# Optimization experiments

Measured on AMD Instinct MI355X. Metric: run time of the kernel, lower is better.

## Reference

```python
import math
import jax, jax.numpy as jnp
import numpy as np

B, T, C = 2, 2048, 2048
H, G = 16, 4
D = C // H  # head_dim = 128
KV = G * D
SOFT_CAP = 50.0
EPS = 1e-6


def setup_inputs() -> dict:
    key = jax.random.key(0)
    ks = jax.random.split(key, 5)
    s = 1.0 / math.sqrt(C)
    return {
        "x": jax.random.normal(ks[0], (B, T, C), jnp.float32),
        "Wq": jax.random.normal(ks[1], (C, C), jnp.float32) * s,
        "Wk": jax.random.normal(ks[2], (KV, C), jnp.float32) * s,
        "Wv": jax.random.normal(ks[3], (KV, C), jnp.float32) * s,
        "Wo": jax.random.normal(ks[4], (C, C), jnp.float32) * s,
        "bo": jnp.zeros((C,), jnp.float32),
        "q_norm_w": jnp.ones((D,), jnp.float32),
        "k_norm_w": jnp.ones((D,), jnp.float32),
    }


def _rmsnorm(x, w):
    # norm/sqrt(d) formulation, eps added to rms (matches torch module exactly)
    rms = jnp.linalg.norm(x, axis=-1, keepdims=True) / math.sqrt(x.shape[-1])
    return w * (x / (rms + EPS))


def _rotary_tables(seq_len, dim):
    inv_freq = 1.0 / (10000.0 ** (jnp.arange(0, dim, 2, dtype=jnp.float32) / dim))
    t = jnp.arange(seq_len, dtype=jnp.float32)
    freqs = jnp.outer(t, inv_freq)  # [T, D/2]
    return jnp.cos(freqs), jnp.sin(freqs)


def _apply_rope(x, cos, sin):
    # x: [B, T, h, D]; cos/sin: [T, D/2] broadcast as [1, T, 1, D/2]
    d = x.shape[-1] // 2
    x1, x2 = x[..., :d], x[..., d:]
    c = cos[None, :, None, :]
    s = sin[None, :, None, :]
    return jnp.concatenate([x1 * c + x2 * s, -x1 * s + x2 * c], axis=-1)


def reference(x, Wq, Wk, Wv, Wo, bo, q_norm_w, k_norm_w):
    b, t, c = x.shape
    q = (x @ Wq.T).reshape(b, t, H, D)
    k = (x @ Wk.T).reshape(b, t, G, D)
    v = (x @ Wv.T).reshape(b, t, G, D)

    cos, sin = _rotary_tables(t, D)
    q = _apply_rope(_rmsnorm(q, q_norm_w), cos, sin)
    k = _apply_rope(_rmsnorm(k, k_norm_w), cos, sin)

    q = q.transpose(0, 2, 1, 3)              # [B, H, T, D]
    k = jnp.repeat(k.transpose(0, 2, 1, 3), H // G, axis=1)  # [B, H, T, D]
    v = jnp.repeat(v.transpose(0, 2, 1, 3), H // G, axis=1)

    att = jnp.einsum("bhqd,bhkd->bhqk", q, k) / math.sqrt(D)
    causal = jnp.tril(jnp.ones((t, t), bool))
    att = jnp.where(causal[None, None], att, -jnp.inf)
    att = SOFT_CAP * jnp.tanh(att / SOFT_CAP)  # masked entries -> -50
    att = jax.nn.softmax(att, axis=-1)

    y = jnp.einsum("bhqk,bhkd->bhqd", att, v)
    y = y.transpose(0, 2, 1, 3).reshape(b, t, c)
    return y @ Wo.T + bo
```

## Files before the change

### kernel.cpp

```cpp
#include <hip/hip_runtime.h>
#include <math.h>

#define T_SEQ 2048
#define C_DIM 2048
#define NH    16
#define NG    4
#define DH    128
#define BATCH 2

typedef unsigned short u16;
typedef __bf16 bf16_t;
typedef bf16_t bf16x8 __attribute__((ext_vector_type(8)));
typedef float  f32x4  __attribute__((ext_vector_type(4)));

static __device__ __forceinline__ u16 f2bf(float f) {
    return __builtin_bit_cast(u16, (__bf16)f);
}

static __device__ __forceinline__ void gll16(const void* g, void* lds) {
    __builtin_amdgcn_global_load_lds(
        (const __attribute__((address_space(1))) void*)(unsigned long long)(g),
        (__attribute__((address_space(3))) void*)(unsigned int)(unsigned long long)(lds),
        16, 0, 0);
}

__global__ __launch_bounds__(256)
void cast_multi(const float* __restrict__ x,  const float* __restrict__ wq,
                const float* __restrict__ wk, const float* __restrict__ wv,
                u16* __restrict__ xo, u16* __restrict__ wqo,
                u16* __restrict__ wko, u16* __restrict__ wvo) {
    int i = blockIdx.x * 256 + threadIdx.x;
    const float* src; u16* dst; int off;
    if (i < 1048576)      { src = x;  dst = xo;  off = i; }
    else if (i < 1572864) { src = wq; dst = wqo; off = i - 1048576; }
    else if (i < 1703936) { src = wk; dst = wko; off = i - 1572864; }
    else                  { src = wv; dst = wvo; off = i - 1703936; }
    const float4* p = (const float4*)src + (size_t)off * 2;
    float4 a = p[0], b = p[1];
    u16 u[8] = {f2bf(a.x), f2bf(a.y), f2bf(a.z), f2bf(a.w),
                f2bf(b.x), f2bf(b.y), f2bf(b.z), f2bf(b.w)};
    *(uint4*)(dst + (size_t)off * 8) = *(const uint4*)u;
}

__global__ __launch_bounds__(256)
void cast_f32_bf16(const float* __restrict__ in, u16* __restrict__ out, int n8) {
    int i = blockIdx.x * 256 + threadIdx.x;
    if (i >= n8) return;
    const float4* p = (const float4*)in + (size_t)i * 2;
    float4 a = p[0], b = p[1];
    u16 u[8] = {f2bf(a.x), f2bf(a.y), f2bf(a.z), f2bf(a.w),
                f2bf(b.x), f2bf(b.y), f2bf(b.z), f2bf(b.w)};
    *(uint4*)(out + (size_t)i * 8) = *(const uint4*)u;
}

__global__ __launch_bounds__(256)
void rope_tables(float* __restrict__ cosT, float* __restrict__ sinT) {
    int i = blockIdx.x * 256 + threadIdx.x;
    int tp = i >> 6, ln = i & 63;
    float invfreq = __builtin_amdgcn_exp2f(-(float)ln * (13.287712379549449f / 64.0f));
    float s, c;
    sincosf((float)tp * invfreq, &s, &c);
    cosT[i] = c;
    sinT[i] = s;
}

static __device__ __forceinline__ void gemm_body(
        u16* As, u16* Bs,
        const u16* __restrict__ A, const u16* __restrict__ B,
        const float* __restrict__ bias, float* __restrict__ C,
        int N, int K, int m0, int n0) {
    const int t    = threadIdx.x;
    const int lane = t & 63, w = t >> 6;
    const int l15  = lane & 15, quad = lane >> 4;
    const int wr   = w >> 1, wc = w & 1;

    f32x4 acc[4][4];
#pragma unroll
    for (int mt = 0; mt < 4; ++mt)
#pragma unroll
        for (int nt = 0; nt < 4; ++nt) acc[mt][nt] = (f32x4){0.f, 0.f, 0.f, 0.f};

    const int off0 = w*2048 + lane*16;
    const int r0 = off0 >> 6,          c0 = (off0 & 63) >> 1;
    const int r1 = (off0+1024) >> 6,   c1 = ((off0+1024) & 63) >> 1;
    const u16* Ag0 = A + (size_t)(m0 + r0) * K + c0;
    const u16* Ag1 = A + (size_t)(m0 + r1) * K + c1;
    const u16* Bg0 = B + (size_t)(n0 + r0) * K + c0;
    const u16* Bg1 = B + (size_t)(n0 + r1) * K + c1;
    char* AsB = (char*)As; char* BsB = (char*)Bs;
    const int ldsOff0 = w*2048, ldsOff1 = w*2048 + 1024;

    for (int k0 = 0; k0 < K; k0 += 32) {
        gll16(Ag0 + k0, AsB + ldsOff0);
        gll16(Ag1 + k0, AsB + ldsOff1);
        gll16(Bg0 + k0, BsB + ldsOff0);
        gll16(Bg1 + k0, BsB + ldsOff1);
        __syncthreads();
        bf16x8 af[4], bf[4];
#pragma unroll
        for (int mt = 0; mt < 4; ++mt)
            af[mt] = __builtin_bit_cast(bf16x8,
                *(const uint4*)&As[(wr*64 + mt*16 + l15)*32 + quad*8]);
#pragma unroll
        for (int nt = 0; nt < 4; ++nt)
            bf[nt] = __builtin_bit_cast(bf16x8,
                *(const uint4*)&Bs[(wc*64 + nt*16 + l15)*32 + quad*8]);
#pragma unroll
        for (int mt = 0; mt < 4; ++mt)
#pragma unroll
            for (int nt = 0; nt < 4; ++nt)
                acc[mt][nt] = __builtin_amdgcn_mfma_f32_16x16x32_bf16(
                                  af[mt], bf[nt], acc[mt][nt], 0, 0, 0);
        __syncthreads();
    }

#pragma unroll
    for (int mt = 0; mt < 4; ++mt)
#pragma unroll
        for (int nt = 0; nt < 4; ++nt) {
            const int col = n0 + wc*64 + nt*16 + l15;
            const float bv = bias ? bias[col] : 0.f;
#pragma unroll
            for (int r = 0; r < 4; ++r) {
                const int row = m0 + wr*64 + mt*16 + quad*4 + r;
                C[(size_t)row * N + col] = acc[mt][nt][r] + bv;
            }
        }
}

__global__ __launch_bounds__(256)
void gemm_nt_bf16(const u16* __restrict__ A, const u16* __restrict__ B,
                  const float* __restrict__ bias, float* __restrict__ C,
                  int N, int K) {
    __shared__ __align__(16) u16 As[128*32];
    __shared__ __align__(16) u16 Bs[128*32];
    gemm_body(As, Bs, A, B, bias, C, N, K, blockIdx.y*128, blockIdx.x*128);
}

__global__ __launch_bounds__(256)
void gemm_qkv(const u16* __restrict__ A,  const u16* __restrict__ Bq,
              const u16* __restrict__ Bk, const u16* __restrict__ Bv,
              float* __restrict__ Cq, float* __restrict__ Ck, float* __restrict__ Cv) {
    __shared__ __align__(16) u16 As[128*32];
    __shared__ __align__(16) u16 Bs[128*32];
    const int bx = blockIdx.x;
    const u16* B; float* C; int N, n0;
    if (bx < 16)      { B = Bq; C = Cq; N = 2048; n0 = bx * 128; }
    else if (bx < 20) { B = Bk; C = Ck; N = 512;  n0 = (bx-16) * 128; }
    else              { B = Bv; C = Cv; N = 512;  n0 = (bx-20) * 128; }
    gemm_body(As, Bs, A, B, nullptr, C, N, 2048, blockIdx.y*128, n0);
}

__global__ __launch_bounds__(256)
void rmsnorm_rope_qk(const float* __restrict__ qf, const float* __restrict__ kf,
                     const float* __restrict__ qw, const float* __restrict__ kw,
                     const float* __restrict__ cosT, const float* __restrict__ sinT,
                     u16* __restrict__ qo, u16* __restrict__ ko) {
    const int blk  = blockIdx.x;
    const int sub  = threadIdx.x >> 6;
    const int lane = threadIdx.x & 63;
    const float* in; const float* w; u16* out; int row, nheads; float scale;
    if (blk < 16384) {
        in = qf; w = qw; out = qo; nheads = NH; scale = 0.08838834764831845f;
        row = blk * 4 + sub;
    } else {
        in = kf; w = kw; out = ko; nheads = NG; scale = 1.0f;
        row = (blk - 16384) * 4 + sub;
    }
    const float* p = in + (size_t)row * 128;
    float x1 = p[lane], x2 = p[lane + 64];
    float ss = x1*x1 + x2*x2;
#pragma unroll
    for (int off = 32; off >= 1; off >>= 1) ss += __shfl_xor(ss, off, 64);
    float inv = 1.0f / (sqrtf(ss * (1.0f/128.0f)) + 1e-6f);
    float x1n = w[lane]      * x1 * inv;
    float x2n = w[lane + 64] * x2 * inv;
    int tpos = (row / nheads) & (T_SEQ - 1);
    float c = cosT[tpos*64 + lane];
    float s = sinT[tpos*64 + lane];
    out[(size_t)row*128 + lane]      = f2bf((x1n * c + x2n * s) * scale);
    out[(size_t)row*128 + lane + 64] = f2bf((x2n * c - x1n * s) * scale);
}

__global__ __launch_bounds__(256)
void v_cast_transpose(const float* __restrict__ v, u16* __restrict__ vt) {
    __shared__ u16 Lt[128 * 66];
    const int t  = threadIdx.x;
    const int t0 = blockIdx.x * 64;
    const int bg = blockIdx.y;
    const int b  = bg / NG, g = bg % NG;
#pragma unroll
    for (int rep = 0; rep < 8; ++rep) {
        int idx = rep * 256 + t;
        int i   = idx >> 5;
        int c   = idx & 31;
        float4 f = *(const float4*)(v + ((size_t)(b*T_SEQ + t0 + i)*NG + g)*DH + c*4);
        Lt[(c*4+0)*66 + i] = f2bf(f.x);
        Lt[(c*4+1)*66 + i] = f2bf(f.y);
        Lt[(c*4+2)*66 + i] = f2bf(f.z);
        Lt[(c*4+3)*66 + i] = f2bf(f.w);
    }
    __syncthreads();
#pragma unroll
    for (int rep = 0; rep < 4; ++rep) {
        int idx = rep * 256 + t;
        int d = idx >> 3, c = idx & 7;
        const u16* src = &Lt[d*66 + c*8];
        uint4 val;
        val.x = *(const unsigned int*)(src + 0);
        val.y = *(const unsigned int*)(src + 2);
        val.z = *(const unsigned int*)(src + 4);
        val.w = *(const unsigned int*)(src + 6);
        *(uint4*)(vt + ((size_t)(bg*DH + d))*T_SEQ + t0 + c*8) = val;
    }
}

__global__ __launch_bounds__(256, 2)
void flash_attn_mfma(const u16* __restrict__ qh, const u16* __restrict__ kh,
                     const u16* __restrict__ vt, u16* __restrict__ y) {
    __shared__ __align__(16) u16 Ks[2][64*128];
    __shared__ __align__(16) u16 Vs[2][128*64];
    __shared__ __align__(16) u16 Ps[64*64];

    const int t    = threadIdx.x;
    const int lane = t & 63, w = t >> 6;
    const int l15  = lane & 15, quad = lane >> 4;
    const int bid  = blockIdx.x;
    const int bg   = bid & 7;
    const int b    = bg >> 2, g = bg & 3;
    const int cidx = bid >> 3;
    const int chunk = b ? cidx : (63 - cidx);
    const int q0   = chunk * 32;
    const int h    = g * (NH / NG) + w;

    const float C0 =  1.4426950408889634f;
    const float C1 = -0.48089834696298777f;
    const float C2 =  0.19235933878519512f;
    const float C3 = -0.07785972536301652f;

    bf16x8 aq[2][4];
#pragma unroll
    for (int m = 0; m < 2; ++m) {
        const u16* qp = qh + ((size_t)(b*T_SEQ + q0 + m*16 + l15) * NH + h) * DH;
#pragma unroll
        for (int kc = 0; kc < 4; ++kc)
            aq[m][kc] = __builtin_bit_cast(bf16x8, *(const uint4*)(qp + kc*32 + quad*8));
    }

    f32x4 accO[2][8];
#pragma unroll
    for (int m = 0; m < 2; ++m)
#pragma unroll
        for (int nd = 0; nd < 8; ++nd) accO[m][nd] = (f32x4){0.f, 0.f, 0.f, 0.f};
    float ls[2][4] = {{0.f,0.f,0.f,0.f},{0.f,0.f,0.f,0.f}};

    const u16* kgb = kh + ((size_t)b*T_SEQ*NG + g)*DH;
    const u16* vgb = vt + ((size_t)(b*NG + g)*DH)*T_SEQ;

    const int krb = t >> 4, kcl = t & 15;
    const int vdb = t >> 3, vcl = t & 7;

    const int ktiles = q0/64 + 1;

#pragma unroll
    for (int j = 0; j < 4; ++j) {
        const int kr = j*16 + krb;
        gll16(kgb + (size_t)kr*(NG*DH) + ((kcl ^ (kr & 7)) << 3),
              (char*)Ks[0] + j*4096 + w*1024);
        const int vd = j*32 + vdb;
        gll16(vgb + (size_t)vd*T_SEQ + ((vcl ^ (vd & 7)) << 3),
              (char*)Vs[0] + j*4096 + w*1024);
    }

    for (int kt = 0; kt < ktiles; ++kt) {
        asm volatile("s_waitcnt vmcnt(0)" ::: "memory");
        __syncthreads();

        if (kt + 1 < ktiles) {
            const int k0n = (kt + 1) * 64, bn = (kt + 1) & 1;
#pragma unroll
            for (int j = 0; j < 4; ++j) {
                const int kr = j*16 + krb;
                gll16(kgb + (size_t)(k0n + kr)*(NG*DH) + ((kcl ^ (kr & 7)) << 3),
                      (char*)Ks[bn] + j*4096 + w*1024);
                const int vd = j*32 + vdb;
                gll16(vgb + (size_t)vd*T_SEQ + k0n + ((vcl ^ (vd & 7)) << 3),
                      (char*)Vs[bn] + j*4096 + w*1024);
            }
        }

        const u16* Kb = Ks[kt & 1];
        const u16* Vb = Vs[kt & 1];
        const int k0 = kt * 64;
        const bool diag = (kt == ktiles - 1);

        f32x4 accS[2][4];
#pragma unroll
        for (int m = 0; m < 2; ++m)
#pragma unroll
            for (int nt = 0; nt < 4; ++nt) accS[m][nt] = (f32x4){0.f,0.f,0.f,0.f};

        __builtin_amdgcn_s_setprio(1);
#pragma unroll
        for (int nt = 0; nt < 4; ++nt) {
            const int krow = nt*16 + l15;
            const int kswz = (krow & 7) << 3;
#pragma unroll
            for (int kc = 0; kc < 4; ++kc) {
                bf16x8 bk = __builtin_bit_cast(bf16x8,
                    *(const uint4*)&Kb[krow*128 + ((kc*32 + quad*8) ^ kswz)]);
                accS[0][nt] = __builtin_amdgcn_mfma_f32_16x16x32_bf16(aq[0][kc], bk, accS[0][nt], 0, 0, 0);
                accS[1][nt] = __builtin_amdgcn_mfma_f32_16x16x32_bf16(aq[1][kc], bk, accS[1][nt], 0, 0, 0);
            }
        }
        __builtin_amdgcn_s_setprio(0);

        bf16x8 ap[2][2];
#pragma unroll
        for (int m = 0; m < 2; ++m) {
#pragma unroll
            for (int nt = 0; nt < 4; ++nt) {
                const int colg = k0 + nt*16 + l15;
#pragma unroll
                for (int r = 0; r < 4; ++r) {
                    float sv = accS[m][nt][r];
                    float z = sv * 0.02f;
                    float u = z * z;
                    float poly = fmaf(u, fmaf(u, fmaf(u, C3, C2), C1), C0);
                    float pv = __builtin_amdgcn_exp2f(sv * poly);
                    if (diag) {
                        const int rowg = q0 + m*16 + quad*4 + r;
                        pv = (colg > rowg) ? 0.f : pv;
                    }
                    ls[m][r] += pv;
                    const int prow = w*16 + r*4 + quad;
                    const int pswz = ((quad << 1) | (r & 1)) << 3;
                    Ps[prow*64 + ((nt*16 + l15) ^ pswz)] = f2bf(pv);
                }
            }
            const int srow = (l15 & 3)*4 + (l15 >> 2);
            const int arow = w*16 + srow;
            const int aswz = (((l15 >> 2) << 1) | (l15 & 1)) << 3;
            ap[m][0] = __builtin_bit_cast(bf16x8,
                *(const uint4*)&Ps[arow*64 + ((quad*8)      ^ aswz)]);
            ap[m][1] = __builtin_bit_cast(bf16x8,
                *(const uint4*)&Ps[arow*64 + ((32 + quad*8) ^ aswz)]);
        }

        __builtin_amdgcn_s_setprio(1);
#pragma unroll
        for (int nd = 0; nd < 8; ++nd) {
            const int vrow = nd*16 + l15;
            const int vswz = (vrow & 7) << 3;
#pragma unroll
            for (int kc = 0; kc < 2; ++kc) {
                bf16x8 bv = __builtin_bit_cast(bf16x8,
                    *(const uint4*)&Vb[vrow*64 + ((kc*32 + quad*8) ^ vswz)]);
                accO[0][nd] = __builtin_amdgcn_mfma_f32_16x16x32_bf16(ap[0][kc], bv, accO[0][nd], 0, 0, 0);
                accO[1][nd] = __builtin_amdgcn_mfma_f32_16x16x32_bf16(ap[1][kc], bv, accO[1][nd], 0, 0, 0);
            }
        }
        __builtin_amdgcn_s_setprio(0);
    }

#pragma unroll
    for (int m = 0; m < 2; ++m)
#pragma unroll
        for (int r = 0; r < 4; ++r) {
            float v = ls[m][r];
            v += __shfl_xor(v, 1, 64);
            v += __shfl_xor(v, 2, 64);
            v += __shfl_xor(v, 4, 64);
            v += __shfl_xor(v, 8, 64);
            const float invl = 1.f / v;
            u16* yp = y + (size_t)(b*T_SEQ + q0 + m*16 + quad*4 + r) * C_DIM + h*DH;
#pragma unroll
            for (int nd = 0; nd < 8; ++nd)
                yp[nd*16 + l15] = f2bf(accO[m][nd][r] * invl);
        }
}

extern "C" void kernel_launch(void* const* d_in, const int* in_sizes, int n_in,
                              void* d_out, int out_size, void* d_ws, size_t ws_size,
                              hipStream_t stream) {
    const float* x  = (const float*)d_in[0];
    const float* Wq = (const float*)d_in[1];
    const float* Wk = (const float*)d_in[2];
    const float* Wv = (const float*)d_in[3];
    const float* Wo = (const float*)d_in[4];
    const float* bo = (const float*)d_in[5];
    const float* qw = (const float*)d_in[6];
    const float* kw = (const float*)d_in[7];
    float* out = (float*)d_out;

    const size_t qE = (size_t)BATCH * T_SEQ * NH * DH;
    const size_t kE = (size_t)BATCH * T_SEQ * NG * DH;
    const size_t wqE = (size_t)C_DIM * C_DIM;
    const size_t wkE = (size_t)(NG*DH) * C_DIM;

    float* qf  = (float*)d_ws;
    float* kf  = qf + qE;
    float* vf  = kf + kE;
    u16*   qh  = (u16*)(vf + kE);
    u16*   khb = qh + qE;
    u16*   vtb = khb + kE;
    u16*   xh  = vtb + kE;
    u16*   wqh = xh + qE;
    u16*   wkh = wqh + wqE;
    u16*   wvh = wkh + wkE;
    float* cosT = (float*)(wvh + wkE);
    float* sinT = cosT + 131072;
    u16*   woh = (u16*)kf;
    u16*   yh  = (u16*)qf;

    const int M = BATCH * T_SEQ;
    dim3 blk(256);

    rope_tables<<<dim3(512), blk, 0, stream>>>(cosT, sinT);

    cast_multi<<<dim3(7168), blk, 0, stream>>>(x, Wq, Wk, Wv, xh, wqh, wkh, wvh);

    gemm_qkv<<<dim3(24, M/128), blk, 0, stream>>>(xh, wqh, wkh, wvh, qf, kf, vf);

    rmsnorm_rope_qk<<<dim3(M*NH/4 + M*NG/4), blk, 0, stream>>>(qf, kf, qw, kw, cosT, sinT, qh, khb);
    v_cast_transpose<<<dim3(T_SEQ/64, BATCH*NG), blk, 0, stream>>>(vf, vtb);

    cast_f32_bf16<<<dim3(wqE/8/256), blk, 0, stream>>>(Wo, woh, wqE/8);

    flash_attn_mfma<<<dim3(512), blk, 0, stream>>>(qh, khb, vtb, yh);

    gemm_nt_bf16<<<dim3(C_DIM/128, M/128), blk, 0, stream>>>(yh, woh, bo, out, C_DIM, C_DIM);
}
```

Measured before the change: 343.8 us.

## Compute transposed S tiles so P stays in registers, removing the LDS round trip

```diff
diff --git a/kernel.cpp b/kernel.cpp
--- a/kernel.cpp
+++ b/kernel.cpp
@@ -220,16 +220,13 @@
                      const u16* __restrict__ vt, u16* __restrict__ y) {
     __shared__ __align__(16) u16 Ks[2][64*128];
     __shared__ __align__(16) u16 Vs[2][128*64];
-    __shared__ __align__(16) u16 Ps[64*64];
 
     const int t    = threadIdx.x;
     const int lane = t & 63, w = t >> 6;
     const int l15  = lane & 15, quad = lane >> 4;
-    const int bid  = blockIdx.x;
-    const int bg   = bid & 7;
+    const int bg   = blockIdx.y;
     const int b    = bg >> 2, g = bg & 3;
-    const int cidx = bid >> 3;
-    const int chunk = b ? cidx : (63 - cidx);
+    const int chunk = b ? (int)blockIdx.x : (63 - (int)blockIdx.x);
     const int q0   = chunk * 32;
     const int h    = g * (NH / NG) + w;
 
@@ -252,7 +249,7 @@
     for (int m = 0; m < 2; ++m)
 #pragma unroll
         for (int nd = 0; nd < 8; ++nd) accO[m][nd] = (f32x4){0.f, 0.f, 0.f, 0.f};
-    float ls[2][4] = {{0.f,0.f,0.f,0.f},{0.f,0.f,0.f,0.f}};
+    float ls[2] = {0.f, 0.f};
 
     const u16* kgb = kh + ((size_t)b*T_SEQ*NG + g)*DH;
     const u16* vgb = vt + ((size_t)(b*NG + g)*DH)*T_SEQ;
@@ -265,7 +262,9 @@
 #pragma unroll
     for (int j = 0; j < 4; ++j) {
         const int kr = j*16 + krb;
-        gll16(kgb + (size_t)kr*(NG*DH) + ((kcl ^ (kr & 7)) << 3),
+        const int rp = kr & 31;
+        const int kphys = (kr & 32) + ((rp >> 2) & 3)*8 + (rp >> 4)*4 + (rp & 3);
+        gll16(kgb + (size_t)kphys*(NG*DH) + ((kcl ^ (kr & 7)) << 3),
               (char*)Ks[0] + j*4096 + w*1024);
         const int vd = j*32 + vdb;
         gll16(vgb + (size_t)vd*T_SEQ + ((vcl ^ (vd & 7)) << 3),
@@ -281,7 +280,9 @@
 #pragma unroll
             for (int j = 0; j < 4; ++j) {
                 const int kr = j*16 + krb;
-                gll16(kgb + (size_t)(k0n + kr)*(NG*DH) + ((kcl ^ (kr & 7)) << 3),
+                const int rp = kr & 31;
+                const int kphys = (kr & 32) + ((rp >> 2) & 3)*8 + (rp >> 4)*4 + (rp & 3);
+                gll16(kgb + (size_t)(k0n + kphys)*(NG*DH) + ((kcl ^ (kr & 7)) << 3),
                       (char*)Ks[bn] + j*4096 + w*1024);
                 const int vd = j*32 + vdb;
                 gll16(vgb + (size_t)vd*T_SEQ + k0n + ((vcl ^ (vd & 7)) << 3),
@@ -294,85 +295,77 @@
         const int k0 = kt * 64;
         const bool diag = (kt == ktiles - 1);
 
-        f32x4 accS[2][4];
-#pragma unroll
-        for (int m = 0; m < 2; ++m)
-#pragma unroll
-            for (int nt = 0; nt < 4; ++nt) accS[m][nt] = (f32x4){0.f,0.f,0.f,0.f};
-
-        __builtin_amdgcn_s_setprio(1);
-#pragma unroll
-        for (int nt = 0; nt < 4; ++nt) {
-            const int krow = nt*16 + l15;
-            const int kswz = (krow & 7) << 3;
-#pragma unroll
-            for (int kc = 0; kc < 4; ++kc) {
-                bf16x8 bk = __builtin_bit_cast(bf16x8,
-                    *(const uint4*)&Kb[krow*128 + ((kc*32 + quad*8) ^ kswz)]);
-                accS[0][nt] = __builtin_amdgcn_mfma_f32_16x16x32_bf16(aq[0][kc], bk, accS[0][nt], 0, 0, 0);
-                accS[1][nt] = __builtin_amdgcn_mfma_f32_16x16x32_bf16(aq[1][kc], bk, accS[1][nt], 0, 0, 0);
-            }
-        }
-        __builtin_amdgcn_s_setprio(0);
-
-        bf16x8 ap[2][2];
-#pragma unroll
-        for (int m = 0; m < 2; ++m) {
-#pragma unroll
-            for (int nt = 0; nt < 4; ++nt) {
-                const int colg = k0 + nt*16 + l15;
-#pragma unroll
-                for (int r = 0; r < 4; ++r) {
-                    float sv = accS[m][nt][r];
-                    float z = sv * 0.02f;
-                    float u = z * z;
-                    float poly = fmaf(u, fmaf(u, fmaf(u, C3, C2), C1), C0);
-                    float pv = __builtin_amdgcn_exp2f(sv * poly);
-                    if (diag) {
-                        const int rowg = q0 + m*16 + quad*4 + r;
-                        pv = (colg > rowg) ? 0.f : pv;
+        bf16x8 pa[2][2];
+#pragma unroll
+        for (int b32 = 0; b32 < 2; ++b32) {
+            alignas(16) u16 pk0[8];
+            alignas(16) u16 pk1[8];
+#pragma unroll
+            for (int sub = 0; sub < 2; ++sub) {
+                const int kc16 = b32*2 + sub;
+                const int krow = kc16*16 + l15;
+                const int kswz = (krow & 7) << 3;
+                f32x4 st0 = (f32x4){0.f,0.f,0.f,0.f};
+                f32x4 st1 = (f32x4){0.f,0.f,0.f,0.f};
+#pragma unroll
+                for (int kc = 0; kc < 4; ++kc) {
+                    bf16x8 ak = __builtin_bit_cast(bf16x8,
+                        *(const uint4*)&Kb[krow*128 + ((kc*32 + quad*8) ^ kswz)]);
+                    st0 = __builtin_amdgcn_mfma_f32_16x16x32_bf16(ak, aq[0][kc], st0, 0, 0, 0);
+                    st1 = __builtin_amdgcn_mfma_f32_16x16x32_bf16(ak, aq[1][kc], st1, 0, 0, 0);
+                }
+#pragma unroll
+                for (int m = 0; m < 2; ++m) {
+                    const f32x4 st = m ? st1 : st0;
+#pragma unroll
+                    for (int r = 0; r < 4; ++r) {
+                        float sv = st[r];
+                        float z = sv * 0.02f;
+                        float u = z * z;
+                        float poly = fmaf(u, fmaf(u, fmaf(u, C3, C2), C1), C0);
+                        float pv = __builtin_amdgcn_exp2f(sv * poly);
+                        if (diag) {
+                            const int keyg = k0 + b32*32 + quad*8 + sub*4 + r;
+                            const int qg   = q0 + m*16 + l15;
+                            pv = (keyg > qg) ? 0.f : pv;
+                        }
+                        ls[m] += pv;
+                        if (m) pk1[sub*4 + r] = f2bf(pv);
+                        else   pk0[sub*4 + r] = f2bf(pv);
                     }
-                    ls[m][r] += pv;
-                    const int prow = w*16 + r*4 + quad;
-                    const int pswz = ((quad << 1) | (r & 1)) << 3;
-                    Ps[prow*64 + ((nt*16 + l15) ^ pswz)] = f2bf(pv);
                 }
             }
-            const int srow = (l15 & 3)*4 + (l15 >> 2);
-            const int arow = w*16 + srow;
-            const int aswz = (((l15 >> 2) << 1) | (l15 & 1)) << 3;
-            ap[m][0] = __builtin_bit_cast(bf16x8,
-                *(const uint4*)&Ps[arow*64 + ((quad*8)      ^ aswz)]);
-            ap[m][1] = __builtin_bit_cast(bf16x8,
-                *(const uint4*)&Ps[arow*64 + ((32 + quad*8) ^ aswz)]);
+            pa[0][b32] = __builtin_bit_cast(bf16x8, *(const uint4*)pk0);
+            pa[1][b32] = __builtin_bit_cast(bf16x8, *(const uint4*)pk1);
         }
 
-        __builtin_amdgcn_s_setprio(1);
 #pragma unroll
         for (int nd = 0; nd < 8; ++nd) {
             const int vrow = nd*16 + l15;
             const int vswz = (vrow & 7) << 3;
 #pragma unroll
-            for (int kc = 0; kc < 2; ++kc) {
+            for (int b32 = 0; b32 < 2; ++b32) {
                 bf16x8 bv = __builtin_bit_cast(bf16x8,
-                    *(const uint4*)&Vb[vrow*64 + ((kc*32 + quad*8) ^ vswz)]);
-                accO[0][nd] = __builtin_amdgcn_mfma_f32_16x16x32_bf16(ap[0][kc], bv, accO[0][nd], 0, 0, 0);
-                accO[1][nd] = __builtin_amdgcn_mfma_f32_16x16x32_bf16(ap[1][kc], bv, accO[1][nd], 0, 0, 0);
+                    *(const uint4*)&Vb[vrow*64 + ((b32*32 + quad*8) ^ vswz)]);
+                accO[0][nd] = __builtin_amdgcn_mfma_f32_16x16x32_bf16(pa[0][b32], bv, accO[0][nd], 0, 0, 0);
+                accO[1][nd] = __builtin_amdgcn_mfma_f32_16x16x32_bf16(pa[1][b32], bv, accO[1][nd], 0, 0, 0);
             }
         }
-        __builtin_amdgcn_s_setprio(0);
+    }
+
+#pragma unroll
+    for (int m = 0; m < 2; ++m) {
+        float v = ls[m];
+        v += __shfl_xor(v, 16, 64);
+        v += __shfl_xor(v, 32, 64);
+        ls[m] = v;
     }
 
 #pragma unroll
     for (int m = 0; m < 2; ++m)
 #pragma unroll
         for (int r = 0; r < 4; ++r) {
-            float v = ls[m][r];
-            v += __shfl_xor(v, 1, 64);
-            v += __shfl_xor(v, 2, 64);
-            v += __shfl_xor(v, 4, 64);
-            v += __shfl_xor(v, 8, 64);
-            const float invl = 1.f / v;
+            const float invl = 1.f / __shfl(ls[m], quad*4 + r, 64);
             u16* yp = y + (size_t)(b*T_SEQ + q0 + m*16 + quad*4 + r) * C_DIM + h*DH;
 #pragma unroll
             for (int nd = 0; nd < 8; ++nd)
@@ -427,7 +420,7 @@
 
     cast_f32_bf16<<<dim3(wqE/8/256), blk, 0, stream>>>(Wo, woh, wqE/8);
 
-    flash_attn_mfma<<<dim3(512), blk, 0, stream>>>(qh, khb, vtb, yh);
+    flash_attn_mfma<<<dim3(T_SEQ/32, BATCH*NG), blk, 0, stream>>>(qh, khb, vtb, yh);
 
     gemm_nt_bf16<<<dim3(C_DIM/128, M/128), blk, 0, stream>>>(yh, woh, bo, out, C_DIM, C_DIM);
 }
```

Measured after the change: 320.8 us. -6.7%, faster.
